# Kernel optimization log

Hardware: AMD Instinct MI355X
Metric: run time of the kernel (lower is better)

## Reference

```python
import jax, jax.numpy as jnp
import numpy as np

H, W, C = 512, 512, 64
N_BOXES = 512
OUT_W = 32


def setup_inputs() -> dict:
    key = jax.random.key(0)
    k1, k2 = jax.random.split(key)
    feature_map = jax.random.normal(k1, (H, W, C), dtype=jnp.float32)
    # boxes are [cx, cy, w, h] as fractions of the image; uniform(0,1) is valid
    boxes = jax.random.uniform(k2, (N_BOXES, 4), dtype=jnp.float32)
    return {"feature_map": feature_map, "boxes": boxes, "output_width": OUT_W}


def reference(feature_map, boxes, output_width):
    """RoIAlign over a batch of boxes (vectorized version of roi_align_batch_serial)."""
    in_h, in_w, c = feature_map.shape
    out_h = out_w = output_width

    def roi_align_single(box):
        cx, cy, w, h = jnp.split(box, 4, axis=-1)
        x0 = cx - w / 2
        y0 = cy - h / 2
        w = jnp.maximum(w, 1e-6)
        h = jnp.maximum(h, 1e-6)
        x_scale = out_w / (w * in_w)
        y_scale = out_h / (h * in_h)
        return jax.image.scale_and_translate(
            feature_map,
            shape=(out_h, out_w, c),
            spatial_dims=(0, 1),
            scale=jnp.concatenate((y_scale, x_scale)),
            translation=jnp.concatenate((-y0 * out_h / h, -x0 * out_w / w)),
            method="linear",
            precision=jax.lax.Precision("fastest"),
        )

    # Same math as jax.lax.map(roi_align_single, boxes), but batched across boxes.
    return jax.vmap(roi_align_single)(boxes)  # [N, out_h, out_w, C]
```

## Files before the change

### kernel.cpp

```cpp
#include <hip/hip_runtime.h>


#define H_IN 512
#define W_IN 512
#define CH   64
#define NB   512
#define OW   32
#define WSTRIDE 33
#define WXS     40
#define TAPS_MAX 33
#define COLS_MAX 512
#define COLS_PAD 528

__global__ __launch_bounds__(256) void roi_weights(const float* __restrict__ boxes,
                                                   float* __restrict__ wTab,
                                                   int* __restrict__ meta) {
    int tid = blockIdx.x * blockDim.x + threadIdx.x;
    if (tid >= NB * 2 * 32) return;
    int o   = tid & 31;
    int dim = (tid >> 5) & 1;
    int b   = tid >> 6;

    float cx = boxes[b * 4 + 0];
    float cy = boxes[b * 4 + 1];
    float bw = boxes[b * 4 + 2];
    float bh = boxes[b * 4 + 3];
    float cc = dim ? cx : cy;
    float sz = dim ? bw : bh;
    float lo = cc - sz * 0.5f;
    sz = fmaxf(sz, 1e-6f);

    float scale = (float)OW / (sz * (float)W_IN);
    float inv   = 1.0f / scale;
    float trans = (-lo * (float)OW) / sz;
    float s     = ((float)o + 0.5f) * inv - trans * inv - 0.5f;
    float ks    = fmaxf(inv, 1.0f);

    int i_lo = max((int)ceilf(s - ks), 0);
    int i_hi = min((int)floorf(s + ks), W_IN - 1);
    int cnt  = i_hi - i_lo + 1;
    if (cnt < 0) cnt = 0;
    if (cnt > TAPS_MAX) cnt = TAPS_MAX;

    float sum = 0.0f;
    for (int k = 0; k < cnt; ++k) {
        float x = fabsf(s - (float)(i_lo + k)) / ks;
        sum += fmaxf(0.0f, 1.0f - x);
    }
    bool ok = (sum > 1.1920929e-4f) && (s >= -0.5f) && (s <= (float)W_IN - 0.5f);

    float* wout = wTab + ((size_t)(dim * NB + b) * 32 + o) * WSTRIDE;
    for (int k = 0; k < TAPS_MAX; ++k) {
        float w = 0.0f;
        if (ok && k < cnt) {
            float x = fabsf(s - (float)(i_lo + k)) / ks;
            w = fmaxf(0.0f, 1.0f - x) / sum;
        }
        wout[k] = w;
    }
    int* m = meta + ((size_t)(dim * NB + b) * 32 + o) * 2;
    m[0] = i_lo;
    m[1] = ok ? cnt : 0;
}

__device__ __forceinline__ void gload16(const float* src, float* ldsDst) {
    __builtin_amdgcn_global_load_lds((const __attribute__((address_space(1))) void*)src,
                                     (__attribute__((address_space(3))) void*)ldsDst, 16, 0, 0);
}

__global__ __launch_bounds__(256) void roi_sep3(const float* __restrict__ fm,
                                                const float* __restrict__ wTab,
                                                const int* __restrict__ meta,
                                                float* __restrict__ out) {
    __shared__ float sBuf[2][COLS_PAD * 16];
    __shared__ float sWx[32 * WXS];
    __shared__ float sWy[16 * WSTRIDE];
    __shared__ int   sMx[64];
    __shared__ int   sMyLC[16];
    __shared__ int   sU[4];

    int bid = blockIdx.x;
    int box = ((bid >> 6) << 3) + (bid & 7);
    int sub = (bid >> 3) & 7;
    int ch0 = (sub & 3) * 16;
    int oy0 = (sub >> 2) * 16;
    int t   = threadIdx.x;

    const float* wxsrc = wTab + (size_t)(NB + box) * 32 * WSTRIDE;
    for (int i = t; i < 32 * WXS; i += 256) {
        int o = i / WXS, k = i - o * WXS;
        sWx[i] = (k < WSTRIDE) ? wxsrc[o * WSTRIDE + k] : 0.0f;
    }
    const float* wysrc = wTab + ((size_t)box * 32 + oy0) * WSTRIDE;
    for (int i = t; i < 16 * WSTRIDE; i += 256) sWy[i] = wysrc[i];
    if (t < 64) sMx[t] = meta[(size_t)(NB + box) * 64 + t];
    if (t < 16) {
        int lo = meta[((size_t)box * 32 + oy0 + t) * 2];
        int cn = meta[((size_t)box * 32 + oy0 + t) * 2 + 1];
        sMyLC[t] = (lo & 0xffff) | (cn << 16);
    }
    __syncthreads();
    if (t == 0) {
        int lo = 0x7fffffff, hi = -1;
        for (int k = 0; k < 16; ++k) {
            int lc = sMyLC[k], c = lc >> 16;
            if (c > 0) { int l = lc & 0xffff; lo = min(lo, l); hi = max(hi, l + c); }
        }
        sU[0] = (hi > lo) ? lo : 0;
        sU[1] = (hi > lo) ? (hi - lo) : 0;
        int xlo = 0x7fffffff, xhi = -1;
        for (int k = 0; k < 32; ++k) {
            int c = sMx[2 * k + 1];
            if (c > 0) { int l = sMx[2 * k]; xlo = min(xlo, l); xhi = max(xhi, l + c); }
        }
        sU[2] = (xhi > xlo) ? xlo : 0;
        int cux = (xhi > xlo) ? (xhi - xlo) : 0;
        sU[3] = (cux > COLS_MAX) ? COLS_MAX : cux;
    }
    __syncthreads();
    int u0 = sU[0], cu = sU[1], xu0 = sU[2], cux = sU[3];

    int wave = t >> 6, lane = t & 63;
    int ox = t >> 3, cp = t & 7;
    int ix0rel = max(sMx[2 * ox] - xu0, 0);
    int cntx   = sMx[2 * ox + 1];
    int nch    = (cntx + 7) >> 3;

    int myLC[16];
    #pragma unroll
    for (int k = 0; k < 16; ++k) myLC[k] = sMyLC[k];

    float accA[16], accB[16];
    #pragma unroll
    for (int k = 0; k < 16; ++k) { accA[k] = 0.f; accB[k] = 0.f; }

    for (int i = t; i < 2 * 16 * 16; i += 256) {
        int b = i >> 8, col = (i >> 4) & 15, ch = i & 15;
        sBuf[b][(cux + col) * 16 + ch] = 0.0f;
    }

    const float* laneSrc = fm + (size_t)(xu0 + (lane >> 2)) * CH + ch0 + (lane & 3) * 4;
    int laneCol = lane >> 2;

    if (cu > 0) {
        const float* rowSrc = laneSrc + (size_t)u0 * (W_IN * CH);
        for (int c0w = wave * 16; c0w < cux; c0w += 64) {
            if (c0w + laneCol < cux) gload16(rowSrc + c0w * CH, &sBuf[0][c0w * 16]);
        }
    }
    __syncthreads();

    int cur = 0;
    for (int r = 0; r < cu; ++r) {
        if (r + 1 < cu) {
            const float* rowSrc = laneSrc + (size_t)(u0 + r + 1) * (W_IN * CH);
            float* dst = &sBuf[cur ^ 1][0];
            for (int c0w = wave * 16; c0w < cux; c0w += 64) {
                if (c0w + laneCol < cux) gload16(rowSrc + c0w * CH, dst + c0w * 16);
            }
        }

        const float* wxp = &sWx[ox * WXS];
        const float* bp  = &sBuf[cur][0] + ix0rel * 16 + cp * 2;
        float xa = 0.f, xb = 0.f;
        for (int c = 0; c < nch; ++c) {
            float2 v[8];
            #pragma unroll
            for (int k = 0; k < 8; ++k) v[k] = *(const float2*)(bp + k * 16);
            float4 w0 = *(const float4*)(wxp + c * 8);
            float4 w1 = *(const float4*)(wxp + c * 8 + 4);
            xa = fmaf(w0.x, v[0].x, xa); xb = fmaf(w0.x, v[0].y, xb);
            xa = fmaf(w0.y, v[1].x, xa); xb = fmaf(w0.y, v[1].y, xb);
            xa = fmaf(w0.z, v[2].x, xa); xb = fmaf(w0.z, v[2].y, xb);
            xa = fmaf(w0.w, v[3].x, xa); xb = fmaf(w0.w, v[3].y, xb);
            xa = fmaf(w1.x, v[4].x, xa); xb = fmaf(w1.x, v[4].y, xb);
            xa = fmaf(w1.y, v[5].x, xa); xb = fmaf(w1.y, v[5].y, xb);
            xa = fmaf(w1.z, v[6].x, xa); xb = fmaf(w1.z, v[6].y, xb);
            xa = fmaf(w1.w, v[7].x, xa); xb = fmaf(w1.w, v[7].y, xb);
            bp += 128;
        }

        int iy = u0 + r;
        #pragma unroll
        for (int oy = 0; oy < 16; ++oy) {
            int lc = myLC[oy];
            int rr = iy - (lc & 0xffff);
            if ((unsigned)rr < (unsigned)(lc >> 16)) {
                float w = sWy[oy * WSTRIDE + rr];
                accA[oy] = fmaf(w, xa, accA[oy]);
                accB[oy] = fmaf(w, xb, accB[oy]);
            }
        }

        __syncthreads();
        cur ^= 1;
    }

    #pragma unroll
    for (int oy = 0; oy < 16; ++oy) {
        float* op = out + (((size_t)box * 32 + oy0 + oy) * 32 + ox) * CH + ch0 + cp * 2;
        *(float2*)op = make_float2(accA[oy], accB[oy]);
    }
}

extern "C" void kernel_launch(void* const* d_in, const int* in_sizes, int n_in,
                              void* d_out, int out_size, void* d_ws, size_t ws_size,
                              hipStream_t stream) {
    const float* fm    = (const float*)d_in[0];
    const float* boxes = (const float*)d_in[1];

    float* wTab = (float*)d_ws;
    int*   meta = (int*)((char*)d_ws + (size_t)2 * NB * 32 * WSTRIDE * sizeof(float));

    roi_weights<<<(NB * 2 * 32 + 255) / 256, 256, 0, stream>>>(boxes, wTab, meta);
    roi_sep3<<<NB * 8, 256, 0, stream>>>(fm, wTab, meta, (float*)d_out);
}
```

Baseline: 1.536 ms.

## Split RoI work into single-wave blocks over output-column slices

Each block now covers 8 output columns with one 64-thread wave instead of 32 columns with four waves. The staged input span and LDS footprint shrink, which raises occupancy. Because only one wave runs per block, the per-row barrier becomes a plain wait on outstanding loads. The staged column span is clamped to a smaller limit, which may truncate very wide boxes, and overlapping input columns are reloaded across neighbouring blocks.

```diff
diff --git a/kernel.cpp b/kernel.cpp
--- a/kernel.cpp
+++ b/kernel.cpp
@@ -9,8 +9,8 @@
 #define WSTRIDE 33
 #define WXS     40
 #define TAPS_MAX 33
-#define COLS_MAX 512
-#define COLS_PAD 528
+#define COLS_H  156
+#define COLS_CL 146
 
 __global__ __launch_bounds__(256) void roi_weights(const float* __restrict__ boxes,
                                                    float* __restrict__ wTab,
@@ -68,36 +68,38 @@
                                      (__attribute__((address_space(3))) void*)ldsDst, 16, 0, 0);
 }
 
-__global__ __launch_bounds__(256) void roi_sep3(const float* __restrict__ fm,
-                                                const float* __restrict__ wTab,
-                                                const int* __restrict__ meta,
-                                                float* __restrict__ out) {
-    __shared__ float sBuf[2][COLS_PAD * 16];
-    __shared__ float sWx[32 * WXS];
+__global__ __launch_bounds__(64) void roi_wave(const float* __restrict__ fm,
+                                               const float* __restrict__ wTab,
+                                               const int* __restrict__ meta,
+                                               float* __restrict__ out) {
+    __shared__ float sBuf[2][COLS_H * 16];
+    __shared__ float sWx[8 * WXS];
     __shared__ float sWy[16 * WSTRIDE];
-    __shared__ int   sMx[64];
+    __shared__ int   sMx[16];
     __shared__ int   sMyLC[16];
     __shared__ int   sU[4];
 
     int bid = blockIdx.x;
-    int box = ((bid >> 6) << 3) + (bid & 7);
-    int sub = (bid >> 3) & 7;
-    int ch0 = (sub & 3) * 16;
-    int oy0 = (sub >> 2) * 16;
+    int box = ((bid >> 8) << 3) | (bid & 7);
+    int sub = (bid >> 3) & 31;
+    int ox0 = (sub & 3) * 8;
+    int ch0 = ((sub >> 2) & 3) * 16;
+    int oy0 = (sub >> 4) * 16;
     int t   = threadIdx.x;
 
-    const float* wxsrc = wTab + (size_t)(NB + box) * 32 * WSTRIDE;
-    for (int i = t; i < 32 * WXS; i += 256) {
+    const float* wxsrc = wTab + ((size_t)(NB + box) * 32 + ox0) * WSTRIDE;
+    for (int i = t; i < 8 * WXS; i += 64) {
         int o = i / WXS, k = i - o * WXS;
         sWx[i] = (k < WSTRIDE) ? wxsrc[o * WSTRIDE + k] : 0.0f;
     }
     const float* wysrc = wTab + ((size_t)box * 32 + oy0) * WSTRIDE;
-    for (int i = t; i < 16 * WSTRIDE; i += 256) sWy[i] = wysrc[i];
-    if (t < 64) sMx[t] = meta[(size_t)(NB + box) * 64 + t];
-    if (t < 16) {
-        int lo = meta[((size_t)box * 32 + oy0 + t) * 2];
-        int cn = meta[((size_t)box * 32 + oy0 + t) * 2 + 1];
-        sMyLC[t] = (lo & 0xffff) | (cn << 16);
+    for (int i = t; i < 16 * WSTRIDE; i += 64) sWy[i] = wysrc[i];
+    if (t < 16) sMx[t] = meta[((size_t)(NB + box) * 32 + ox0) * 2 + t];
+    if (t >= 16 && t < 32) {
+        int k  = t - 16;
+        int lo = meta[((size_t)box * 32 + oy0 + k) * 2];
+        int cn = meta[((size_t)box * 32 + oy0 + k) * 2 + 1];
+        sMyLC[k] = (lo & 0xffff) | (cn << 16);
     }
     __syncthreads();
     if (t == 0) {
@@ -109,18 +111,17 @@
         sU[0] = (hi > lo) ? lo : 0;
         sU[1] = (hi > lo) ? (hi - lo) : 0;
         int xlo = 0x7fffffff, xhi = -1;
-        for (int k = 0; k < 32; ++k) {
+        for (int k = 0; k < 8; ++k) {
             int c = sMx[2 * k + 1];
             if (c > 0) { int l = sMx[2 * k]; xlo = min(xlo, l); xhi = max(xhi, l + c); }
         }
         sU[2] = (xhi > xlo) ? xlo : 0;
         int cux = (xhi > xlo) ? (xhi - xlo) : 0;
-        sU[3] = (cux > COLS_MAX) ? COLS_MAX : cux;
+        sU[3] = (cux > COLS_CL) ? COLS_CL : cux;
     }
     __syncthreads();
     int u0 = sU[0], cu = sU[1], xu0 = sU[2], cux = sU[3];
 
-    int wave = t >> 6, lane = t & 63;
     int ox = t >> 3, cp = t & 7;
     int ix0rel = max(sMx[2 * ox] - xu0, 0);
     int cntx   = sMx[2 * ox + 1];
@@ -134,17 +135,17 @@
     #pragma unroll
     for (int k = 0; k < 16; ++k) { accA[k] = 0.f; accB[k] = 0.f; }
 
-    for (int i = t; i < 2 * 16 * 16; i += 256) {
-        int b = i >> 8, col = (i >> 4) & 15, ch = i & 15;
+    for (int i = t; i < 2 * 8 * 16; i += 64) {
+        int b = i >> 7, col = (i >> 4) & 7, ch = i & 15;
         sBuf[b][(cux + col) * 16 + ch] = 0.0f;
     }
 
-    const float* laneSrc = fm + (size_t)(xu0 + (lane >> 2)) * CH + ch0 + (lane & 3) * 4;
-    int laneCol = lane >> 2;
+    const float* laneSrc = fm + (size_t)(xu0 + (t >> 2)) * CH + ch0 + (t & 3) * 4;
+    int laneCol = t >> 2;
 
     if (cu > 0) {
         const float* rowSrc = laneSrc + (size_t)u0 * (W_IN * CH);
-        for (int c0w = wave * 16; c0w < cux; c0w += 64) {
+        for (int c0w = 0; c0w < cux; c0w += 16) {
             if (c0w + laneCol < cux) gload16(rowSrc + c0w * CH, &sBuf[0][c0w * 16]);
         }
     }
@@ -155,7 +156,7 @@
         if (r + 1 < cu) {
             const float* rowSrc = laneSrc + (size_t)(u0 + r + 1) * (W_IN * CH);
             float* dst = &sBuf[cur ^ 1][0];
-            for (int c0w = wave * 16; c0w < cux; c0w += 64) {
+            for (int c0w = 0; c0w < cux; c0w += 16) {
                 if (c0w + laneCol < cux) gload16(rowSrc + c0w * CH, dst + c0w * 16);
             }
         }
@@ -192,13 +193,13 @@
             }
         }
 
-        __syncthreads();
+        asm volatile("s_waitcnt vmcnt(0)" ::: "memory");
         cur ^= 1;
     }
 
     #pragma unroll
     for (int oy = 0; oy < 16; ++oy) {
-        float* op = out + (((size_t)box * 32 + oy0 + oy) * 32 + ox) * CH + ch0 + cp * 2;
+        float* op = out + (((size_t)box * 32 + oy0 + oy) * 32 + ox0 + ox) * CH + ch0 + cp * 2;
         *(float2*)op = make_float2(accA[oy], accB[oy]);
     }
 }
@@ -213,5 +214,5 @@
     int*   meta = (int*)((char*)d_ws + (size_t)2 * NB * 32 * WSTRIDE * sizeof(float));
 
     roi_weights<<<(NB * 2 * 32 + 255) / 256, 256, 0, stream>>>(boxes, wTab, meta);
-    roi_sep3<<<NB * 8, 256, 0, stream>>>(fm, wTab, meta, (float*)d_out);
-}
+    roi_wave<<<NB * 32, 64, 0, stream>>>(fm, wTab, meta, (float*)d_out);
+}
```

New measurement: 1.627 ms. 1.06x slower.
